# Performance work log

Measured on AMD Instinct MI355X. Metric: run time of the kernel, lower is better.

Reference implementation:

```python
import jax, jax.numpy as jnp
import numpy as np

HEADS = 4
OUT_CH = 64
NEG_SLOPE = 0.2  # PyG GATConv default negative_slope


def setup_inputs() -> dict:
    key = jax.random.key(0)
    k1, k2, k3, k4, k5, k6 = jax.random.split(key, 6)
    N, E, IN_CH = 50000, 800000, 128
    x = jax.random.normal(k1, (N, IN_CH), dtype=jnp.float32)
    edge_index = jax.random.randint(k2, (2, E), 0, N, dtype=jnp.int64)
    # Learned parameters (glorot-style init)
    s_w = (6.0 / (IN_CH + HEADS * OUT_CH)) ** 0.5
    W = jax.random.uniform(k3, (IN_CH, HEADS * OUT_CH), minval=-s_w, maxval=s_w, dtype=jnp.float32)
    s_a = (6.0 / (1 + OUT_CH)) ** 0.5
    att_src = jax.random.uniform(k4, (HEADS, OUT_CH), minval=-s_a, maxval=s_a, dtype=jnp.float32)
    att_dst = jax.random.uniform(k5, (HEADS, OUT_CH), minval=-s_a, maxval=s_a, dtype=jnp.float32)
    bias = jnp.zeros((HEADS * OUT_CH,), dtype=jnp.float32)
    return {"x": x, "W": W, "att_src": att_src, "att_dst": att_dst, "bias": bias, "edge_index": edge_index}


def reference(x, W, att_src, att_dst, bias, edge_index):
    # Faithful GATConv (PyG defaults: add_self_loops=True, concat=True, eval mode => no dropout)
    N = x.shape[0]
    loops = jnp.arange(N, dtype=edge_index.dtype)
    src = jnp.concatenate([edge_index[0], loops])  # message source j
    dst = jnp.concatenate([edge_index[1], loops])  # message target i

    xp = (x @ W).reshape(N, HEADS, OUT_CH)          # [N, H, C]
    a_src = jnp.einsum('nhc,hc->nh', xp, att_src)   # [N, H]
    a_dst = jnp.einsum('nhc,hc->nh', xp, att_dst)   # [N, H]

    alpha = jax.nn.leaky_relu(a_src[src] + a_dst[dst], NEG_SLOPE)  # [E', H]
    # segment softmax over incoming edges of each target node
    amax = jax.ops.segment_max(alpha, dst, num_segments=N)
    ex = jnp.exp(alpha - jax.lax.stop_gradient(amax)[dst])
    denom = jax.ops.segment_sum(ex, dst, num_segments=N)
    coef = ex / denom[dst]                           # [E', H]

    msg = xp[src] * coef[:, :, None]                 # [E', H, C]
    out = jax.ops.segment_sum(msg, dst, num_segments=N)  # [N, H, C]
    return out.reshape(N, HEADS * OUT_CH) + bias
```

## Files before the change

### kernel.cpp

```cpp
#include <hip/hip_runtime.h>

#define HEADS 4
#define OUTC 64
#define INC 128
#define HC 256
#define NEG 0.2f

typedef __attribute__((ext_vector_type(8))) short bf16x8;
typedef __attribute__((ext_vector_type(4))) float f32x4;

static __device__ __forceinline__ float bf2f(unsigned short u){
  unsigned int x = ((unsigned int)u) << 16;
  return __uint_as_float(x);
}
static __device__ __forceinline__ unsigned short f2bf(float f){
  unsigned int x = __float_as_uint(f);
  unsigned int lsb = (x >> 16) & 1u;
  x += 0x7fffu + lsb;
  return (unsigned short)(x >> 16);
}
static __device__ __forceinline__ void split8(float4 a, float4 b, bf16x8& hi, bf16x8& lo){
  float v[8] = {a.x, a.y, a.z, a.w, b.x, b.y, b.z, b.w};
  #pragma unroll
  for (int i = 0; i < 8; ++i){
    unsigned short h = f2bf(v[i]);
    hi[i] = (short)h;
    lo[i] = (short)f2bf(v[i] - bf2f(h));
  }
}

__global__ void k_conv_e_hist(const int* __restrict__ ei,
                              int* __restrict__ srcc, int* __restrict__ dstc,
                              int* __restrict__ pos, int* __restrict__ deg, int E){
  int e = blockIdx.x * 256 + threadIdx.x;
  bool valid = (e < E);
  int ee = valid ? e : 0;
  int hiw = ei[2 * ee + 1];
  bool hz = valid ? (hiw == 0) : true;
  unsigned long long mask = __ballot(hz);
  bool i64 = (mask == ~0ULL);
  int s, d;
  if (i64){ s = ei[2 * ee]; d = ei[2 * (size_t)E + 2 * ee]; }
  else    { s = ei[ee];     d = ei[(size_t)E + ee]; }
  if (valid){
    srcc[e] = s; dstc[e] = d;
    pos[e] = atomicAdd(&deg[d], 1);
  }
}

__global__ void k_split_w(const float* __restrict__ W, unsigned short* __restrict__ Wthi,
                          unsigned short* __restrict__ Wtlo){
  int t = blockIdx.x * 256 + threadIdx.x;
  int k = t >> 8, n = t & 255;
  float v = W[t];
  unsigned short hi = f2bf(v);
  Wthi[n * INC + k] = hi;
  Wtlo[n * INC + k] = f2bf(v - bf2f(hi));
}

__global__ __launch_bounds__(256) void k_gemm_fused(const float* __restrict__ X,
    const unsigned short* __restrict__ Wthi, const unsigned short* __restrict__ Wtlo,
    const float* __restrict__ att_src, const float* __restrict__ att_dst,
    unsigned short* __restrict__ XPh, float* __restrict__ a_src, float* __restrict__ a_dst,
    int N){
  int w = threadIdx.x >> 6, lane = threadIdx.x & 63;
  int m0 = blockIdx.x * 64;
  int quad = lane >> 4;
  int l15 = lane & 15;
  int colg[4];
  #pragma unroll
  for (int t = 0; t < 4; ++t) colg[t] = w * 64 + t * 16 + l15;

  bool rv[4]; int rowr[4];
  #pragma unroll
  for (int rt = 0; rt < 4; ++rt){
    rv[rt] = (m0 + rt * 16) < N;
    rowr[rt] = rv[rt] ? (m0 + rt * 16 + l15) : 0;
  }

  f32x4 acc[4][4];
  #pragma unroll
  for (int rt = 0; rt < 4; ++rt)
    #pragma unroll
    for (int t = 0; t < 4; ++t) acc[rt][t] = (f32x4){0.f, 0.f, 0.f, 0.f};

  #pragma unroll
  for (int kk = 0; kk < 4; ++kk){
    float4 va[4], vb[4];
    #pragma unroll
    for (int rt = 0; rt < 4; ++rt){
      const float* xr = X + (size_t)rowr[rt] * INC + kk * 32 + quad * 8;
      va[rt] = *(const float4*)xr;
      vb[rt] = *(const float4*)(xr + 4);
    }
    bf16x8 bh[4], bl[4];
    #pragma unroll
    for (int t = 0; t < 4; ++t){
      size_t bo = (size_t)colg[t] * INC + kk * 32 + quad * 8;
      bh[t] = *(const bf16x8*)(Wthi + bo);
      bl[t] = *(const bf16x8*)(Wtlo + bo);
    }
    bf16x8 ah[4], al[4];
    #pragma unroll
    for (int rt = 0; rt < 4; ++rt) split8(va[rt], vb[rt], ah[rt], al[rt]);
    #pragma unroll
    for (int rt = 0; rt < 4; ++rt){
      #pragma unroll
      for (int t = 0; t < 4; ++t){
        acc[rt][t] = __builtin_amdgcn_mfma_f32_16x16x32_bf16(ah[rt], bh[t], acc[rt][t], 0, 0, 0);
        acc[rt][t] = __builtin_amdgcn_mfma_f32_16x16x32_bf16(ah[rt], bl[t], acc[rt][t], 0, 0, 0);
        acc[rt][t] = __builtin_amdgcn_mfma_f32_16x16x32_bf16(al[rt], bh[t], acc[rt][t], 0, 0, 0);
      }
    }
  }

  #pragma unroll
  for (int rt = 0; rt < 4; ++rt){
    if (!rv[rt]) continue;
    #pragma unroll
    for (int t = 0; t < 4; ++t){
      #pragma unroll
      for (int r = 0; r < 4; ++r){
        XPh[(size_t)(m0 + rt * 16 + quad * 4 + r) * HC + colg[t]] = f2bf(acc[rt][t][r]);
      }
    }
  }

  float as[4], ad[4];
  #pragma unroll
  for (int t = 0; t < 4; ++t){
    as[t] = att_src[colg[t]];
    ad[t] = att_dst[colg[t]];
  }
  #pragma unroll
  for (int rt = 0; rt < 4; ++rt){
    if (!rv[rt]) continue;
    float ps[4], pd[4];
    #pragma unroll
    for (int r = 0; r < 4; ++r){
      ps[r] = acc[rt][0][r] * as[0] + acc[rt][1][r] * as[1]
            + acc[rt][2][r] * as[2] + acc[rt][3][r] * as[3];
      pd[r] = acc[rt][0][r] * ad[0] + acc[rt][1][r] * ad[1]
            + acc[rt][2][r] * ad[2] + acc[rt][3][r] * ad[3];
    }
    #pragma unroll
    for (int msk = 1; msk < 16; msk <<= 1){
      #pragma unroll
      for (int r = 0; r < 4; ++r){
        ps[r] += __shfl_xor(ps[r], msk, 64);
        pd[r] += __shfl_xor(pd[r], msk, 64);
      }
    }
    if (l15 == 0){
      #pragma unroll
      for (int r = 0; r < 4; ++r){
        int n = m0 + rt * 16 + quad * 4 + r;
        a_src[n * HEADS + w] = ps[r];
        a_dst[n * HEADS + w] = pd[r];
      }
    }
  }
}

__global__ __launch_bounds__(256) void k_scan1(const int* __restrict__ deg,
                                               int* __restrict__ out,
                                               int* __restrict__ bsum, int N){
  __shared__ int tsum[256];
  int t = threadIdx.x;
  int base = blockIdx.x * 1024 + t * 4;
  int v[4]; int s = 0;
  #pragma unroll
  for (int k = 0; k < 4; ++k){ int i = base + k; v[k] = (i < N) ? deg[i] : 0; s += v[k]; }
  tsum[t] = s;
  __syncthreads();
  for (int off = 1; off < 256; off <<= 1){
    int x = (t >= off) ? tsum[t - off] : 0;
    __syncthreads();
    tsum[t] += x;
    __syncthreads();
  }
  int excl = tsum[t] - s;
  if (t == 255) bsum[blockIdx.x] = tsum[255];
  int run = excl;
  #pragma unroll
  for (int k = 0; k < 4; ++k){ int i = base + k; if (i < N) out[i] = run; run += v[k]; }
}

__global__ __launch_bounds__(256) void k_scan23(int* __restrict__ rowstart,
                                                const int* __restrict__ bsum,
                                                int N, int E){
  int lane = threadIdx.x & 63;
  int partial = 0;
  for (int i = lane; i < blockIdx.x; i += 64) partial += bsum[i];
  #pragma unroll
  for (int msk = 32; msk; msk >>= 1) partial += __shfl_xor(partial, msk, 64);
  int base = blockIdx.x * 1024 + threadIdx.x * 4;
  #pragma unroll
  for (int k = 0; k < 4; ++k){ int i = base + k; if (i < N) rowstart[i] += partial; }
  if (blockIdx.x == 0 && threadIdx.x == 0) rowstart[N] = E;
}

__global__ void k_scatter(const int* __restrict__ srcc, const int* __restrict__ dstc,
                          const int* __restrict__ pos, const int* __restrict__ rowstart,
                          int* __restrict__ csr, int E){
  int e = blockIdx.x * 256 + threadIdx.x;
  if (e < E){
    int d = dstc[e];
    csr[rowstart[d] + pos[e]] = srcc[e];
  }
}

__global__ __launch_bounds__(256) void k_fused(const unsigned short* __restrict__ XPh,
    const float* __restrict__ a_src, const float* __restrict__ a_dst,
    const int* __restrict__ rowstart, const int* __restrict__ csr,
    const float* __restrict__ bias, float* __restrict__ out, int N){
  __shared__ float sh[4][64][4];
  int w = threadIdx.x >> 6, lane = threadIdx.x & 63;
  int n = blockIdx.x * 4 + w;
  bool alive = (n < N);
  if (!alive) n = 0;
  int r0 = rowstart[n], r1 = rowstart[n + 1];
  int deg = r1 - r0;
  int total = deg + 1;
  int h = lane >> 4;
  float4 ad4 = *(const float4*)&a_dst[n * HEADS];
  bool fast = (total <= 64);
  int jv = n;
  float msel = 0.f, inv_sel = 0.f;

  if (fast){
    if (lane < deg) jv = csr[r0 + lane];
    float l0 = -1e30f, l1 = -1e30f, l2 = -1e30f, l3 = -1e30f;
    if (lane < total){
      float4 a4 = *(const float4*)&a_src[jv * HEADS];
      l0 = a4.x + ad4.x; l0 = (l0 > 0.f) ? l0 : NEG * l0;
      l1 = a4.y + ad4.y; l1 = (l1 > 0.f) ? l1 : NEG * l1;
      l2 = a4.z + ad4.z; l2 = (l2 > 0.f) ? l2 : NEG * l2;
      l3 = a4.w + ad4.w; l3 = (l3 > 0.f) ? l3 : NEG * l3;
    }
    float p0 = __expf(l0), p1 = __expf(l1), p2 = __expf(l2), p3 = __expf(l3);
    float s0 = p0, s1 = p1, s2 = p2, s3 = p3;
    #pragma unroll
    for (int msk = 32; msk; msk >>= 1){
      s0 += __shfl_xor(s0, msk, 64);
      s1 += __shfl_xor(s1, msk, 64);
      s2 += __shfl_xor(s2, msk, 64);
      s3 += __shfl_xor(s3, msk, 64);
    }
    if (lane < total){
      sh[w][lane][0] = p0 / s0;
      sh[w][lane][1] = p1 / s1;
      sh[w][lane][2] = p2 / s2;
      sh[w][lane][3] = p3 / s3;
    }
  } else {
    float m[4] = {-1e30f, -1e30f, -1e30f, -1e30f};
    float s[4] = {0.f, 0.f, 0.f, 0.f};
    float adArr[4] = {ad4.x, ad4.y, ad4.z, ad4.w};
    for (int e = lane; e < total; e += 64){
      int j = (e < deg) ? csr[r0 + e] : n;
      float4 a4 = *(const float4*)&a_src[j * HEADS];
      float aa[4] = {a4.x, a4.y, a4.z, a4.w};
      #pragma unroll
      for (int hh = 0; hh < 4; ++hh){
        float l = aa[hh] + adArr[hh];
        l = (l > 0.f) ? l : NEG * l;
        if (l > m[hh]){ s[hh] = s[hh] * __expf(m[hh] - l) + 1.f; m[hh] = l; }
        else            s[hh] += __expf(l - m[hh]);
      }
    }
    #pragma unroll
    for (int hh = 0; hh < 4; ++hh){
      float mm = m[hh], ss = s[hh];
      #pragma unroll
      for (int msk = 32; msk; msk >>= 1){
        float m2 = __shfl_xor(mm, msk, 64);
        float s2 = __shfl_xor(ss, msk, 64);
        float M = fmaxf(mm, m2);
        float ns = 0.f;
        if (mm > -1e29f) ns += ss * __expf(mm - M);
        if (m2 > -1e29f) ns += s2 * __expf(m2 - M);
        mm = M; ss = ns;
      }
      m[hh] = mm; s[hh] = ss;
    }
    msel    = (h == 0) ? m[0] : (h == 1) ? m[1] : (h == 2) ? m[2] : m[3];
    inv_sel = 1.f / ((h == 0) ? s[0] : (h == 1) ? s[1] : (h == 2) ? s[2] : s[3]);
  }

  __syncthreads();

  float a0 = 0.f, a1 = 0.f, a2 = 0.f, a3 = 0.f;
  const unsigned short* xb = XPh + lane * 4;
  if (fast){
    int e = 0;
    for (; e + 8 <= total; e += 8){
      int jj[8]; float cf[8]; ushort4 xv[8];
      #pragma unroll
      for (int q = 0; q < 8; ++q){
        jj[q] = __builtin_amdgcn_readlane(jv, e + q);
        cf[q] = sh[w][e + q][h];
      }
      #pragma unroll
      for (int q = 0; q < 8; ++q) xv[q] = *(const ushort4*)(xb + (size_t)jj[q] * HC);
      #pragma unroll
      for (int q = 0; q < 8; ++q){
        a0 += cf[q] * bf2f(xv[q].x); a1 += cf[q] * bf2f(xv[q].y);
        a2 += cf[q] * bf2f(xv[q].z); a3 += cf[q] * bf2f(xv[q].w);
      }
    }
    for (; e < total; ++e){
      int j = __builtin_amdgcn_readlane(jv, e);
      float c = sh[w][e][h];
      ushort4 xv = *(const ushort4*)(xb + (size_t)j * HC);
      a0 += c * bf2f(xv.x); a1 += c * bf2f(xv.y); a2 += c * bf2f(xv.z); a3 += c * bf2f(xv.w);
    }
  } else {
    float adh = (h == 0) ? ad4.x : (h == 1) ? ad4.y : (h == 2) ? ad4.z : ad4.w;
    for (int e = 0; e < total; ++e){
      int j = (e < deg) ? csr[r0 + e] : n;
      float4 a4 = *(const float4*)&a_src[j * HEADS];
      float ah = (h == 0) ? a4.x : (h == 1) ? a4.y : (h == 2) ? a4.z : a4.w;
      float l = ah + adh;
      l = (l > 0.f) ? l : NEG * l;
      float c = __expf(l - msel) * inv_sel;
      ushort4 xv = *(const ushort4*)(xb + (size_t)j * HC);
      a0 += c * bf2f(xv.x); a1 += c * bf2f(xv.y); a2 += c * bf2f(xv.z); a3 += c * bf2f(xv.w);
    }
  }
  if (alive){
    float4 b4 = *(const float4*)&bias[lane * 4];
    float4 r; r.x = a0 + b4.x; r.y = a1 + b4.y; r.z = a2 + b4.z; r.w = a3 + b4.w;
    *(float4*)&out[(size_t)n * HC + lane * 4] = r;
  }
}

extern "C" void kernel_launch(void* const* d_in, const int* in_sizes, int n_in,
                              void* d_out, int out_size, void* d_ws, size_t ws_size,
                              hipStream_t stream){
  const float* x       = (const float*)d_in[0];
  const float* W       = (const float*)d_in[1];
  const float* att_src = (const float*)d_in[2];
  const float* att_dst = (const float*)d_in[3];
  const float* bias    = (const float*)d_in[4];
  const int*   ei      = (const int*)d_in[5];
  int N = in_sizes[0] / INC;
  int E = in_sizes[5] / 2;

  char* p = (char*)d_ws;
  auto alloc = [&](size_t bytes)->char*{
    char* r = p; p += (bytes + 255) & ~(size_t)255; return r;
  };
  unsigned short* Wthi = (unsigned short*)alloc((size_t)INC * HC * 2);
  unsigned short* Wtlo = (unsigned short*)alloc((size_t)INC * HC * 2);
  unsigned short* XPh  = (unsigned short*)alloc((size_t)N * HC * 2);
  float* aSrc          = (float*)alloc((size_t)N * HEADS * 4);
  float* aDst          = (float*)alloc((size_t)N * HEADS * 4);
  int* deg             = (int*)alloc((size_t)N * 4);
  int* rowstart        = (int*)alloc(((size_t)N + 1) * 4);
  int* srcc            = (int*)alloc((size_t)E * 4);
  int* dstc            = (int*)alloc((size_t)E * 4);
  int* pos             = (int*)alloc((size_t)E * 4);
  int* csr             = (int*)alloc((size_t)E * 4);
  int* bsum            = (int*)alloc(256 * 4);

  hipMemsetAsync(deg, 0, (size_t)N * 4, stream);
  k_conv_e_hist<<<(E + 255) / 256, 256, 0, stream>>>(ei, srcc, dstc, pos, deg, E);

  k_split_w<<<(INC * HC) / 256, 256, 0, stream>>>(W, Wthi, Wtlo);
  k_gemm_fused<<<(N + 63) / 64, 256, 0, stream>>>(x, Wthi, Wtlo, att_src, att_dst,
                                                  XPh, aSrc, aDst, N);

  int nb = (N + 1023) / 1024;
  k_scan1<<<nb, 256, 0, stream>>>(deg, rowstart, bsum, N);
  k_scan23<<<nb, 256, 0, stream>>>(rowstart, bsum, N, E);
  k_scatter<<<(E + 255) / 256, 256, 0, stream>>>(srcc, dstc, pos, rowstart, csr, E);

  k_fused<<<(N + 3) / 4, 256, 0, stream>>>(XPh, aSrc, aDst, rowstart, csr, bias,
                                           (float*)d_out, N);
}
```

Measured before the change: 250.2 us.

## Fuse CSR build and weight split into one persistent grid-barrier kernel

Replaces the edge histogram, weight split, two-pass scan and scatter kernels with one persistent kernel of 256 blocks. Each thread keeps its edges' source, destination and slot in registers across software grid barriers. This removes several launches and the global round trips through the srcc, dstc and pos arrays. Separately, the fast path of the aggregation kernel drops its block-wide __syncthreads and pads its edge loop to a multiple of eight using zero coefficients, removing the scalar tail loop. The cost is that the persistent kernel relies on all blocks being co-resident and caps edges at 13×65536 and nodes at 65536.

```diff
diff --git a/kernel.cpp b/kernel.cpp
--- a/kernel.cpp
+++ b/kernel.cpp
@@ -5,6 +5,9 @@
 #define INC 128
 #define HC 256
 #define NEG 0.2f
+#define NB 256
+#define TPB 256
+#define MAXE 13
 
 typedef __attribute__((ext_vector_type(8))) short bf16x8;
 typedef __attribute__((ext_vector_type(4))) float f32x4;
@@ -29,33 +32,80 @@
   }
 }
 
-__global__ void k_conv_e_hist(const int* __restrict__ ei,
-                              int* __restrict__ srcc, int* __restrict__ dstc,
-                              int* __restrict__ pos, int* __restrict__ deg, int E){
-  int e = blockIdx.x * 256 + threadIdx.x;
-  bool valid = (e < E);
-  int ee = valid ? e : 0;
-  int hiw = ei[2 * ee + 1];
-  bool hz = valid ? (hiw == 0) : true;
-  unsigned long long mask = __ballot(hz);
-  bool i64 = (mask == ~0ULL);
-  int s, d;
-  if (i64){ s = ei[2 * ee]; d = ei[2 * (size_t)E + 2 * ee]; }
-  else    { s = ei[ee];     d = ei[(size_t)E + ee]; }
-  if (valid){
-    srcc[e] = s; dstc[e] = d;
-    pos[e] = atomicAdd(&deg[d], 1);
-  }
-}
-
-__global__ void k_split_w(const float* __restrict__ W, unsigned short* __restrict__ Wthi,
-                          unsigned short* __restrict__ Wtlo){
-  int t = blockIdx.x * 256 + threadIdx.x;
-  int k = t >> 8, n = t & 255;
-  float v = W[t];
-  unsigned short hi = f2bf(v);
-  Wthi[n * INC + k] = hi;
-  Wtlo[n * INC + k] = f2bf(v - bf2f(hi));
+static __device__ __forceinline__ void gbar(int* bar, int idx, int nblocks){
+  __syncthreads();
+  if (threadIdx.x == 0){
+    __threadfence();
+    __hip_atomic_fetch_add(&bar[idx], 1, __ATOMIC_RELEASE, __HIP_MEMORY_SCOPE_AGENT);
+    while (__hip_atomic_load(&bar[idx], __ATOMIC_ACQUIRE, __HIP_MEMORY_SCOPE_AGENT) < nblocks){}
+    __threadfence();
+  }
+  __syncthreads();
+}
+
+__global__ __launch_bounds__(256) void k_csr(const int* __restrict__ ei,
+    const float* __restrict__ W, unsigned short* __restrict__ Wthi,
+    unsigned short* __restrict__ Wtlo, int* __restrict__ deg,
+    int* __restrict__ rowstart, int* __restrict__ bsumG, int* __restrict__ csr,
+    int* bar, int N, int E){
+  int tid = threadIdx.x, b = blockIdx.x;
+  int tg = b * TPB + tid;
+
+  if (tg < 32768){
+    int k = tg >> 8, n = tg & 255;
+    float v = W[tg];
+    unsigned short hi = f2bf(v);
+    Wthi[n * INC + k] = hi;
+    Wtlo[n * INC + k] = f2bf(v - bf2f(hi));
+  }
+
+  int se[MAXE], de[MAXE], pe[MAXE];
+  #pragma unroll
+  for (int it = 0; it < MAXE; ++it){
+    int e = tg + it * (NB * TPB);
+    bool valid = (e < E);
+    int ee = valid ? e : 0;
+    int hiw = ei[2 * ee + 1];
+    bool hz = valid ? (hiw == 0) : true;
+    unsigned long long mask = __ballot(hz);
+    bool i64 = (mask == ~0ULL);
+    int s, d;
+    if (i64){ s = ei[2 * ee]; d = ei[2 * (size_t)E + 2 * ee]; }
+    else    { s = ei[ee];     d = ei[(size_t)E + ee]; }
+    se[it] = s; de[it] = d;
+    pe[it] = valid ? atomicAdd(&deg[d], 1) : 0;
+  }
+  gbar(bar, 0, NB);
+
+  __shared__ int tsum[TPB];
+  int i0 = b * TPB + tid;
+  int v = (i0 < N) ? deg[i0] : 0;
+  tsum[tid] = v;
+  __syncthreads();
+  for (int off = 1; off < TPB; off <<= 1){
+    int x = (tid >= off) ? tsum[tid - off] : 0;
+    __syncthreads();
+    tsum[tid] += x;
+    __syncthreads();
+  }
+  if (i0 < N) rowstart[i0] = tsum[tid] - v;
+  if (tid == TPB - 1) bsumG[b] = tsum[TPB - 1];
+  gbar(bar, 1, NB);
+
+  int lane = tid & 63;
+  int partial = 0;
+  for (int i = lane; i < b; i += 64) partial += bsumG[i];
+  #pragma unroll
+  for (int msk = 32; msk; msk >>= 1) partial += __shfl_xor(partial, msk, 64);
+  if (i0 < N) rowstart[i0] += partial;
+  if (tg == 0) rowstart[N] = E;
+  gbar(bar, 2, NB);
+
+  #pragma unroll
+  for (int it = 0; it < MAXE; ++it){
+    int e = tg + it * (NB * TPB);
+    if (e < E) csr[rowstart[de[it]] + pe[it]] = se[it];
+  }
 }
 
 __global__ __launch_bounds__(256) void k_gemm_fused(const float* __restrict__ X,
@@ -159,54 +209,6 @@
         a_dst[n * HEADS + w] = pd[r];
       }
     }
-  }
-}
-
-__global__ __launch_bounds__(256) void k_scan1(const int* __restrict__ deg,
-                                               int* __restrict__ out,
-                                               int* __restrict__ bsum, int N){
-  __shared__ int tsum[256];
-  int t = threadIdx.x;
-  int base = blockIdx.x * 1024 + t * 4;
-  int v[4]; int s = 0;
-  #pragma unroll
-  for (int k = 0; k < 4; ++k){ int i = base + k; v[k] = (i < N) ? deg[i] : 0; s += v[k]; }
-  tsum[t] = s;
-  __syncthreads();
-  for (int off = 1; off < 256; off <<= 1){
-    int x = (t >= off) ? tsum[t - off] : 0;
-    __syncthreads();
-    tsum[t] += x;
-    __syncthreads();
-  }
-  int excl = tsum[t] - s;
-  if (t == 255) bsum[blockIdx.x] = tsum[255];
-  int run = excl;
-  #pragma unroll
-  for (int k = 0; k < 4; ++k){ int i = base + k; if (i < N) out[i] = run; run += v[k]; }
-}
-
-__global__ __launch_bounds__(256) void k_scan23(int* __restrict__ rowstart,
-                                                const int* __restrict__ bsum,
-                                                int N, int E){
-  int lane = threadIdx.x & 63;
-  int partial = 0;
-  for (int i = lane; i < blockIdx.x; i += 64) partial += bsum[i];
-  #pragma unroll
-  for (int msk = 32; msk; msk >>= 1) partial += __shfl_xor(partial, msk, 64);
-  int base = blockIdx.x * 1024 + threadIdx.x * 4;
-  #pragma unroll
-  for (int k = 0; k < 4; ++k){ int i = base + k; if (i < N) rowstart[i] += partial; }
-  if (blockIdx.x == 0 && threadIdx.x == 0) rowstart[N] = E;
-}
-
-__global__ void k_scatter(const int* __restrict__ srcc, const int* __restrict__ dstc,
-                          const int* __restrict__ pos, const int* __restrict__ rowstart,
-                          int* __restrict__ csr, int E){
-  int e = blockIdx.x * 256 + threadIdx.x;
-  if (e < E){
-    int d = dstc[e];
-    csr[rowstart[d] + pos[e]] = srcc[e];
   }
 }
 
@@ -228,6 +230,9 @@
   int jv = n;
   float msel = 0.f, inv_sel = 0.f;
 
+  float a0 = 0.f, a1 = 0.f, a2 = 0.f, a3 = 0.f;
+  const unsigned short* xb = XPh + lane * 4;
+
   if (fast){
     if (lane < deg) jv = csr[r0 + lane];
     float l0 = -1e30f, l1 = -1e30f, l2 = -1e30f, l3 = -1e30f;
@@ -247,11 +252,25 @@
       s2 += __shfl_xor(s2, msk, 64);
       s3 += __shfl_xor(s3, msk, 64);
     }
-    if (lane < total){
-      sh[w][lane][0] = p0 / s0;
-      sh[w][lane][1] = p1 / s1;
-      sh[w][lane][2] = p2 / s2;
-      sh[w][lane][3] = p3 / s3;
+    sh[w][lane][0] = p0 / s0;
+    sh[w][lane][1] = p1 / s1;
+    sh[w][lane][2] = p2 / s2;
+    sh[w][lane][3] = p3 / s3;
+    int tot8 = (total + 7) & ~7;
+    for (int e = 0; e < tot8; e += 8){
+      int jj[8]; float cf[8]; ushort4 xv[8];
+      #pragma unroll
+      for (int q = 0; q < 8; ++q){
+        jj[q] = __builtin_amdgcn_readlane(jv, e + q);
+        cf[q] = sh[w][e + q][h];
+      }
+      #pragma unroll
+      for (int q = 0; q < 8; ++q) xv[q] = *(const ushort4*)(xb + (size_t)jj[q] * HC);
+      #pragma unroll
+      for (int q = 0; q < 8; ++q){
+        a0 += cf[q] * bf2f(xv[q].x); a1 += cf[q] * bf2f(xv[q].y);
+        a2 += cf[q] * bf2f(xv[q].z); a3 += cf[q] * bf2f(xv[q].w);
+      }
     }
   } else {
     float m[4] = {-1e30f, -1e30f, -1e30f, -1e30f};
@@ -286,36 +305,6 @@
     }
     msel    = (h == 0) ? m[0] : (h == 1) ? m[1] : (h == 2) ? m[2] : m[3];
     inv_sel = 1.f / ((h == 0) ? s[0] : (h == 1) ? s[1] : (h == 2) ? s[2] : s[3]);
-  }
-
-  __syncthreads();
-
-  float a0 = 0.f, a1 = 0.f, a2 = 0.f, a3 = 0.f;
-  const unsigned short* xb = XPh + lane * 4;
-  if (fast){
-    int e = 0;
-    for (; e + 8 <= total; e += 8){
-      int jj[8]; float cf[8]; ushort4 xv[8];
-      #pragma unroll
-      for (int q = 0; q < 8; ++q){
-        jj[q] = __builtin_amdgcn_readlane(jv, e + q);
-        cf[q] = sh[w][e + q][h];
-      }
-      #pragma unroll
-      for (int q = 0; q < 8; ++q) xv[q] = *(const ushort4*)(xb + (size_t)jj[q] * HC);
-      #pragma unroll
-      for (int q = 0; q < 8; ++q){
-        a0 += cf[q] * bf2f(xv[q].x); a1 += cf[q] * bf2f(xv[q].y);
-        a2 += cf[q] * bf2f(xv[q].z); a3 += cf[q] * bf2f(xv[q].w);
-      }
-    }
-    for (; e < total; ++e){
-      int j = __builtin_amdgcn_readlane(jv, e);
-      float c = sh[w][e][h];
-      ushort4 xv = *(const ushort4*)(xb + (size_t)j * HC);
-      a0 += c * bf2f(xv.x); a1 += c * bf2f(xv.y); a2 += c * bf2f(xv.z); a3 += c * bf2f(xv.w);
-    }
-  } else {
     float adh = (h == 0) ? ad4.x : (h == 1) ? ad4.y : (h == 2) ? ad4.z : ad4.w;
     for (int e = 0; e < total; ++e){
       int j = (e < deg) ? csr[r0 + e] : n;
@@ -356,26 +345,18 @@
   unsigned short* XPh  = (unsigned short*)alloc((size_t)N * HC * 2);
   float* aSrc          = (float*)alloc((size_t)N * HEADS * 4);
   float* aDst          = (float*)alloc((size_t)N * HEADS * 4);
-  int* deg             = (int*)alloc((size_t)N * 4);
+  int* degbar          = (int*)alloc(((size_t)N + 16) * 4);
+  int* deg             = degbar;
+  int* bar             = degbar + N;
   int* rowstart        = (int*)alloc(((size_t)N + 1) * 4);
-  int* srcc            = (int*)alloc((size_t)E * 4);
-  int* dstc            = (int*)alloc((size_t)E * 4);
-  int* pos             = (int*)alloc((size_t)E * 4);
   int* csr             = (int*)alloc((size_t)E * 4);
-  int* bsum            = (int*)alloc(256 * 4);
-
-  hipMemsetAsync(deg, 0, (size_t)N * 4, stream);
-  k_conv_e_hist<<<(E + 255) / 256, 256, 0, stream>>>(ei, srcc, dstc, pos, deg, E);
-
-  k_split_w<<<(INC * HC) / 256, 256, 0, stream>>>(W, Wthi, Wtlo);
+  int* bsumG           = (int*)alloc(NB * 4);
+
+  hipMemsetAsync(degbar, 0, ((size_t)N + 16) * 4, stream);
+  k_csr<<<NB, TPB, 0, stream>>>(ei, W, Wthi, Wtlo, deg, rowstart, bsumG, csr,
+                                bar, N, E);
   k_gemm_fused<<<(N + 63) / 64, 256, 0, stream>>>(x, Wthi, Wtlo, att_src, att_dst,
                                                   XPh, aSrc, aDst, N);
-
-  int nb = (N + 1023) / 1024;
-  k_scan1<<<nb, 256, 0, stream>>>(deg, rowstart, bsum, N);
-  k_scan23<<<nb, 256, 0, stream>>>(rowstart, bsum, N, E);
-  k_scatter<<<(E + 255) / 256, 256, 0, stream>>>(srcc, dstc, pos, rowstart, csr, E);
-
   k_fused<<<(N + 3) / 4, 256, 0, stream>>>(XPh, aSrc, aDst, rowstart, csr, bias,
                                            (float*)d_out, N);
 }
```

Result: slower. 312.4 us (+24.9%).
